# Optimization experiments

Measured on AMD Instinct MI355X. Metric: run time of the kernel, lower is better.

The kernel has to match this reference:

```python
import jax, jax.numpy as jnp
import numpy as np

NH = 16  # num_heads from init_kwargs


def setup_inputs() -> dict:
    key = jax.random.key(0)
    ks = jax.random.split(key, 7)
    B, L, S, H = 4, 2, 1024, 1024
    s = 0.02  # weight init scale to keep logits numerically tame
    return {
        "x": jax.random.normal(ks[0], (B, S, H), jnp.float32),
        "y": jax.random.normal(ks[1], (L, B, S, H), jnp.float32),
        "bias": jax.random.normal(ks[2], (B, 1, 1, S), jnp.float32),
        "Wq": jax.random.normal(ks[3], (H, H), jnp.float32) * s,
        "Wk": jax.random.normal(ks[4], (L, H, H), jnp.float32) * s,
        "Wv": jax.random.normal(ks[5], (L, H, H), jnp.float32) * s,
        "Wo": jax.random.normal(ks[6], (H, H), jnp.float32) * s,
    }


def reference(x, y, bias, Wq, Wk, Wv, Wo):
    # x: [B, Lq, H]; y: [L, B, Lk, H] (stacked list of per-link memories)
    B, Lq, H = x.shape
    L, _, Lk, _ = y.shape
    d = H // NH

    # shared query projection, split heads: [B, NH, Lq, d], pre-scaled
    q = (x @ Wq).reshape(B, Lq, NH, d).transpose(0, 2, 1, 3) * (d ** -0.5)

    # per-link K/V projections, split heads -> [B, L, NH, Lk, d]
    kp = jnp.einsum('lbsh,lhe->lbse', y, Wk).reshape(L, B, Lk, NH, d).transpose(1, 0, 3, 2, 4)
    vp = jnp.einsum('lbsh,lhe->lbse', y, Wv).reshape(L, B, Lk, NH, d).transpose(1, 0, 3, 2, 4)

    # per-link logits [B, L, NH, Lq, Lk] + broadcast bias (concat across links == broadcast)
    logits = jnp.einsum('bhqd,blhkd->blhqk', q, kp) + bias[:, None]

    # computation_mode == 1: joint softmax over the link-summed logits
    joint = logits.sum(axis=1)                # [B, NH, Lq, Lk]
    w = jax.nn.softmax(joint, axis=-1)        # (training=False -> no dropout)

    # sum_l (w @ v_l) == w @ sum_l v_l  (w is shared across links)
    ctx = jnp.einsum('bhqk,bhkd->bhqd', w, vp.sum(axis=1))

    # combine heads [B, Lq, H] and output projection
    out = ctx.transpose(0, 2, 1, 3).reshape(B, Lq, H) @ Wo
    return out
```

## Files before the change

### kernel.cpp

```cpp
#include <hip/hip_runtime.h>
#include <cstdint>

typedef __bf16 bf16_t;
typedef bf16_t bf16x4 __attribute__((ext_vector_type(4)));
typedef bf16_t bf16x8 __attribute__((ext_vector_type(8)));
typedef float f32x4 __attribute__((ext_vector_type(4)));

#define GLD_LDS16(g, l)                                                        \
  __builtin_amdgcn_global_load_lds(                                            \
      (const __attribute__((address_space(1))) void*)(g),                      \
      (__attribute__((address_space(3))) void*)(l), 16, 0, 0)

#define LOG2E 1.44269504088896340736f

static __device__ __forceinline__ unsigned short bf16_bits(float f) {
  bf16_t h = (bf16_t)f;
  return __builtin_bit_cast(unsigned short, h);
}

__global__ void prep_kernel(const float* __restrict__ x,
                            const float* __restrict__ y,
                            const float* __restrict__ Wq,
                            const float* __restrict__ Wk,
                            const float* __restrict__ Wv,
                            const float* __restrict__ Wo,
                            bf16_t* __restrict__ xb, bf16_t* __restrict__ yb,
                            bf16_t* __restrict__ WqT,
                            bf16_t* __restrict__ WkvT,
                            bf16_t* __restrict__ WoT) {
  __shared__ float tile[32][33];
  int bid = blockIdx.x;
  if (bid < 6144) {
    int i = bid * 256 + threadIdx.x;
    const float* src;
    bf16_t* dst;
    if (i < 524288) { src = x; dst = xb; }
    else            { src = y; dst = yb; i -= 524288; }
    const float4* s = (const float4*)src;
    float4 a = s[i * 2];
    float4 b = s[i * 2 + 1];
    bf16x8 o;
    o[0] = (bf16_t)a.x; o[1] = (bf16_t)a.y; o[2] = (bf16_t)a.z; o[3] = (bf16_t)a.w;
    o[4] = (bf16_t)b.x; o[5] = (bf16_t)b.y; o[6] = (bf16_t)b.z; o[7] = (bf16_t)b.w;
    *(bf16x8*)(dst + (size_t)i * 8) = o;
    return;
  }
  bid -= 6144;
  const float* src; bf16_t* dst; int R, lb;
  if (bid < 1024)      { src = Wq; dst = WqT;                        R = 1024; lb = bid; }
  else if (bid < 3072) { src = Wk; dst = WkvT;                       R = 2048; lb = bid - 1024; }
  else if (bid < 5120) { src = Wv; dst = WkvT + (size_t)1024 * 2048; R = 2048; lb = bid - 3072; }
  else                 { src = Wo; dst = WoT;                        R = 1024; lb = bid - 5120; }
  int c0 = (lb & 31) << 5, r0 = (lb >> 5) << 5;
  int tc = threadIdx.x & 31, tr = threadIdx.x >> 5;
#pragma unroll
  for (int i = 0; i < 4; i++)
    tile[tr + i * 8][tc] = src[(size_t)(r0 + tr + i * 8) * 1024 + c0 + tc];
  __syncthreads();
#pragma unroll
  for (int i = 0; i < 4; i++)
    dst[(size_t)(c0 + tr + i * 8) * R + r0 + tc] = (bf16_t)tile[tc][tr + i * 8];
}


#define GEMM_STAGE(buf, kt)                                                    \
  {                                                                            \
    const int kbase = (kt) * 32;                                               \
    int kg0 = kbase + ak0;                                                     \
    const bf16_t* s0 = (kg0 < Ksplit)                                          \
                           ? (A0 + (size_t)(m0 + ar0) * 1024 + kg0)            \
                           : (A1 + (size_t)(m0 + ar0) * 1024 + (kg0 - Ksplit));\
    GLD_LDS16(s0, As[buf] + c0 * 8);                                           \
    int kg1 = kbase + ak1;                                                     \
    const bf16_t* s1 = (kg1 < Ksplit)                                          \
                           ? (A0 + (size_t)(m0 + ar1) * 1024 + kg1)            \
                           : (A1 + (size_t)(m0 + ar1) * 1024 + (kg1 - Ksplit));\
    GLD_LDS16(s1, As[buf] + c1 * 8);                                           \
    const bf16_t* b0 = BT + (size_t)(n0 + ar0) * Ktot + kbase + ak0;           \
    GLD_LDS16(b0, Bs[buf] + c0 * 8);                                           \
    const bf16_t* b1 = BT + (size_t)(n0 + ar1) * Ktot + kbase + ak1;           \
    GLD_LDS16(b1, Bs[buf] + c1 * 8);                                           \
  }

#define GEMM_DECLS                                                             \
  const int t = threadIdx.x, w = t >> 6, l = t & 63;                           \
  const int l15 = l & 15, l4 = l >> 4;                                         \
  const int wr = w >> 1, wc = w & 1;                                           \
  const int c0 = t, c1 = t + 256;                                              \
  const int ar0 = c0 >> 2, ar1 = c1 >> 2;                                      \
  const int ak0 = ((c0 & 3) ^ ((ar0 >> 1) & 3)) * 8;                           \
  const int ak1 = ((c1 & 3) ^ ((ar1 >> 1) & 3)) * 8;                           \
  int offA[4], offB[4];                                                        \
  _Pragma("unroll") for (int mi = 0; mi < 4; mi++) {                           \
    int rA = wr * 64 + mi * 16 + l15;                                          \
    offA[mi] = rA * 32 + (l4 ^ ((rA >> 1) & 3)) * 8;                           \
    int rB = wc * 64 + mi * 16 + l15;                                          \
    offB[mi] = rB * 32 + (l4 ^ ((rB >> 1) & 3)) * 8;                           \
  }

#define GEMM_MAINLOOP                                                          \
  GEMM_STAGE(0, 0);                                                            \
  __syncthreads();                                                             \
  int cur = 0;                                                                 \
  for (int kt = 0; kt < nkt; ++kt) {                                           \
    if (kt + 1 < nkt) GEMM_STAGE(cur ^ 1, kt + 1);                             \
    bf16x8 af[4], bfr[4];                                                      \
    _Pragma("unroll") for (int mi = 0; mi < 4; mi++)                           \
        af[mi] = *(const bf16x8*)&As[cur][offA[mi]];                           \
    _Pragma("unroll") for (int ni = 0; ni < 4; ni++)                           \
        bfr[ni] = *(const bf16x8*)&Bs[cur][offB[ni]];                          \
    _Pragma("unroll") for (int mi = 0; mi < 4; mi++)                           \
        _Pragma("unroll") for (int ni = 0; ni < 4; ni++)                       \
            acc[mi][ni] = __builtin_amdgcn_mfma_f32_16x16x32_bf16(             \
                af[mi], bfr[ni], acc[mi][ni], 0, 0, 0);                        \
    __syncthreads();                                                           \
    cur ^= 1;                                                                  \
  }

__global__ __launch_bounds__(256, 2) void qkv_kernel(
    const bf16_t* __restrict__ xbp, const bf16_t* __restrict__ ybp,
    const bf16_t* __restrict__ WqT, const bf16_t* __restrict__ WkvT,
    bf16_t* __restrict__ Qb, bf16_t* __restrict__ Kb,
    bf16_t* __restrict__ VTb) {
  __shared__ bf16_t As[2][128 * 32];
  __shared__ bf16_t Bs[2][128 * 32];
  GEMM_DECLS
  const bool isQ = blockIdx.x < 256;
  const int i = isQ ? blockIdx.x : blockIdx.x - 256;
  const int ybt = (i & 7) * 4 + ((i >> 3) & 3);
  const int xbt = i >> 5;
  const int m0 = ybt * 128, n0 = xbt * 128;
  const bf16_t* A0 = isQ ? xbp : ybp;
  const bf16_t* A1 = isQ ? xbp : ybp + (size_t)4096 * 1024;
  const int Ksplit = 1024;
  const bf16_t* BT = isQ ? WqT : WkvT;
  const int Ktot = isQ ? 1024 : 2048;
  const int nkt = Ktot >> 5;
  f32x4 acc[4][4] = {};

  GEMM_MAINLOOP

#pragma unroll
  for (int mi = 0; mi < 4; mi++) {
#pragma unroll
    for (int ni = 0; ni < 4; ni++) {
      const int rbase = m0 + wr * 64 + mi * 16 + l4 * 4;
      const int col = n0 + wc * 64 + ni * 16 + l15;
      if (isQ) {
#pragma unroll
        for (int rr = 0; rr < 4; rr++)
          Qb[(size_t)(rbase + rr) * 1024 + col] =
              (bf16_t)(acc[mi][ni][rr] * (0.125f * LOG2E));
      } else if (n0 < 1024) {
#pragma unroll
        for (int rr = 0; rr < 4; rr++)
          Kb[(size_t)(rbase + rr) * 1024 + col] = (bf16_t)acc[mi][ni][rr];
      } else {
        union { unsigned short u[4]; uint2 v; } pk;
#pragma unroll
        for (int rr = 0; rr < 4; rr++)
          pk.u[rr] = bf16_bits(acc[mi][ni][rr]);
        *(uint2*)&VTb[(size_t)(col - 1024) * 4096 + rbase] = pk.v;
      }
    }
  }
}

__global__ __launch_bounds__(256, 2) void gemm_o(const bf16_t* __restrict__ A0,
                                                 const bf16_t* __restrict__ BT,
                                                 float* __restrict__ Cp) {
  __shared__ bf16_t As[2][128 * 32];
  __shared__ bf16_t Bs[2][128 * 32];
  GEMM_DECLS
  const int i = blockIdx.x;
  const int ybt = (i & 7) * 4 + ((i >> 3) & 3);
  const int xbt = i >> 5;
  const int m0 = ybt * 128, n0 = xbt * 128;
  const bf16_t* A1 = A0;
  const int Ksplit = 1024, Ktot = 1024, nkt = 32;
  f32x4 acc[4][4] = {};

  GEMM_MAINLOOP

#pragma unroll
  for (int mi = 0; mi < 4; mi++) {
#pragma unroll
    for (int ni = 0; ni < 4; ni++) {
      const int rbase = m0 + wr * 64 + mi * 16 + l4 * 4;
      const int col = n0 + wc * 64 + ni * 16 + l15;
#pragma unroll
      for (int rr = 0; rr < 4; rr++)
        Cp[(size_t)(rbase + rr) * 1024 + col] = acc[mi][ni][rr];
    }
  }
}

__global__ __launch_bounds__(256, 4) void attn_kernel(
    const bf16_t* __restrict__ Q, const bf16_t* __restrict__ K,
    const bf16_t* __restrict__ VT, const float* __restrict__ bias,
    bf16_t* __restrict__ ctx) {
  __shared__ bf16_t Ks[2][64 * 64];
  __shared__ bf16_t Vs[2][64 * 64];
  __shared__ bf16_t Ps[4][1024];
  const int t = threadIdx.x, w = t >> 6, l = t & 63;
  const int l15 = l & 15, l4 = l >> 4;
  const int id = blockIdx.x;
  const int bh = id & 63, qt = id >> 6;
  const int b = bh >> 4, h = bh & 15;

  bf16x8 qf[2];
  {
    const bf16_t* Qb =
        Q + (size_t)(b * 1024 + qt * 64 + w * 16 + l15) * 1024 + h * 64;
#pragma unroll
    for (int ks = 0; ks < 2; ks++)
      qf[ks] = *(const bf16x8*)&Qb[ks * 32 + l4 * 8];
  }

#define ATTN_STAGE(buf, kt)                                                    \
  {                                                                            \
    _Pragma("unroll") for (int j = 0; j < 2; j++) {                            \
      int c = t + j * 256;                                                     \
      int row = c >> 3, sl = (c & 7) ^ (row & 7);                              \
      const bf16_t* srck =                                                     \
          K + (size_t)(b * 1024 + (kt) * 64 + row) * 1024 + h * 64 + sl * 8;   \
      GLD_LDS16(srck, Ks[buf] + c * 8);                                        \
      const bf16_t* srcv =                                                     \
          VT + (size_t)(h * 64 + row) * 4096 + b * 1024 + (kt) * 64 + sl * 8;  \
      GLD_LDS16(srcv, Vs[buf] + c * 8);                                        \
    }                                                                          \
  }

  float mrun = -INFINITY, lrun = 0.f;
  f32x4 ctxacc[4] = {};

  ATTN_STAGE(0, 0);
  __syncthreads();
  int cur = 0;
  for (int kt = 0; kt < 16; ++kt) {
    if (kt + 1 < 16) ATTN_STAGE(cur ^ 1, kt + 1);

    f32x4 sacc[4] = {};
#pragma unroll
    for (int ks = 0; ks < 2; ks++) {
#pragma unroll
      for (int ni = 0; ni < 4; ni++) {
        int krow = ni * 16 + l15;
        int eoff = (krow * 64 + ks * 32 + l4 * 8) ^ ((krow & 7) << 3);
        bf16x8 kf = *(const bf16x8*)&Ks[cur][eoff];
        sacc[ni] = __builtin_amdgcn_mfma_f32_16x16x32_bf16(kf, qf[ks],
                                                           sacc[ni], 0, 0, 0);
      }
    }
#pragma unroll
    for (int ni = 0; ni < 4; ni++) {
      float4 bb =
          *(const float4*)&bias[b * 1024 + kt * 64 + ni * 16 + l4 * 4];
      sacc[ni][0] += (2.0f * LOG2E) * bb.x;
      sacc[ni][1] += (2.0f * LOG2E) * bb.y;
      sacc[ni][2] += (2.0f * LOG2E) * bb.z;
      sacc[ni][3] += (2.0f * LOG2E) * bb.w;
    }
    float tm = -INFINITY;
#pragma unroll
    for (int ni = 0; ni < 4; ni++)
#pragma unroll
      for (int rr = 0; rr < 4; rr++) tm = fmaxf(tm, sacc[ni][rr]);
    tm = fmaxf(tm, __shfl_xor(tm, 16));
    tm = fmaxf(tm, __shfl_xor(tm, 32));
    float mnew = fmaxf(mrun, tm);
    float sc = exp2f(mrun - mnew);
    float rsum = 0.f;
#pragma unroll
    for (int ni = 0; ni < 4; ni++) {
      bf16x4 pk;
#pragma unroll
      for (int rr = 0; rr < 4; rr++) {
        float p = exp2f(sacc[ni][rr] - mnew);
        rsum += p;
        pk[rr] = (bf16_t)p;
      }
      *(bf16x4*)&Ps[w][(ni * 2 + (l4 >> 1)) * 128 + l15 * 8 + (l4 & 1) * 4] =
          pk;
    }
    rsum += __shfl_xor(rsum, 16);
    rsum += __shfl_xor(rsum, 32);
    lrun = lrun * sc + rsum;
    mrun = mnew;
#pragma unroll
    for (int ni = 0; ni < 4; ni++) ctxacc[ni] *= sc;
#pragma unroll
    for (int kk = 0; kk < 2; kk++) {
      bf16x8 pf = *(const bf16x8*)&Ps[w][(kk * 4 + l4) * 128 + l15 * 8];
#pragma unroll
      for (int ni = 0; ni < 4; ni++) {
        int drow = ni * 16 + l15;
        int voff = (drow * 64 + kk * 32 + l4 * 8) ^ ((drow & 7) << 3);
        bf16x8 vf = *(const bf16x8*)&Vs[cur][voff];
        ctxacc[ni] = __builtin_amdgcn_mfma_f32_16x16x32_bf16(vf, pf, ctxacc[ni],
                                                             0, 0, 0);
      }
    }
    __syncthreads();
    cur ^= 1;
  }

  bf16_t* T = Ks[0];
  {
    float inv = 1.0f / lrun;
    int q = w * 16 + l15;
#pragma unroll
    for (int ni = 0; ni < 4; ni++) {
      bf16x4 tv;
#pragma unroll
      for (int rr = 0; rr < 4; rr++) tv[rr] = (bf16_t)(ctxacc[ni][rr] * inv);
      int d0 = ni * 16 + l4 * 4;
      *(bf16x4*)&T[q * 64 + (d0 ^ ((l15 & 7) << 3))] = tv;
    }
  }
  __syncthreads();
#pragma unroll
  for (int c = t; c < 512; c += 256) {
    int row = c >> 3, col8 = c & 7;
    bf16x8 v = *(const bf16x8*)&T[row * 64 + ((col8 * 8) ^ ((row & 7) << 3))];
    *(bf16x8*)&ctx[(size_t)(b * 1024 + qt * 64 + row) * 1024 + h * 64 +
                   col8 * 8] = v;
  }
#undef ATTN_STAGE
}

extern "C" void kernel_launch(void* const* d_in, const int* in_sizes, int n_in,
                              void* d_out, int out_size, void* d_ws,
                              size_t ws_size, hipStream_t stream) {
  const float* x = (const float*)d_in[0];
  const float* y = (const float*)d_in[1];
  const float* bias = (const float*)d_in[2];
  const float* Wq = (const float*)d_in[3];
  const float* Wk = (const float*)d_in[4];
  const float* Wv = (const float*)d_in[5];
  const float* Wo = (const float*)d_in[6];
  float* out = (float*)d_out;

  char* ws = (char*)d_ws;
  const size_t MB = 1024 * 1024;
  bf16_t* xb   = (bf16_t*)(ws + 0 * MB);
  bf16_t* yb   = (bf16_t*)(ws + 8 * MB);
  bf16_t* WqT  = (bf16_t*)(ws + 24 * MB);
  bf16_t* WkvT = (bf16_t*)(ws + 26 * MB);
  bf16_t* WoT  = (bf16_t*)(ws + 34 * MB);
  bf16_t* Qb   = (bf16_t*)(ws + 36 * MB);
  bf16_t* Kb   = (bf16_t*)(ws + 44 * MB);
  bf16_t* VTb  = (bf16_t*)(ws + 52 * MB);
  bf16_t* ctxb = (bf16_t*)(ws + 60 * MB);

  prep_kernel<<<12288, 256, 0, stream>>>(x, y, Wq, Wk, Wv, Wo, xb, yb, WqT,
                                         WkvT, WoT);
  qkv_kernel<<<768, 256, 0, stream>>>(xb, yb, WqT, WkvT, Qb, Kb, VTb);
  attn_kernel<<<1024, 256, 0, stream>>>(Qb, Kb, VTb, bias, ctxb);
  gemm_o<<<256, 256, 0, stream>>>(ctxb, WoT, out);
}
```

Baseline: 137.8 us.

## Switch attention to 32x32x16 MFMA with register-resident P via permlane swap

Rewrites the attention kernel to use 32x32x16 bf16 MFMA tiles, with each wave handling 32 query rows and a block covering 128 queries, so the grid is halved. The softmax probabilities are packed to bf16 with v_cvt_pk_bf16_f32 and rearranged across lane halves with v_permlane32_swap. This removes the LDS round trip for P and the extra shuffles for the row max and sum. The trade-off is higher register pressure (launch bounds lowered to 2 blocks) and fewer blocks in flight.

Measured after the change: 141.6 us. +2.7%, slower.

```diff
diff --git a/kernel.cpp b/kernel.cpp
--- a/kernel.cpp
+++ b/kernel.cpp
@@ -5,6 +5,7 @@
 typedef bf16_t bf16x4 __attribute__((ext_vector_type(4)));
 typedef bf16_t bf16x8 __attribute__((ext_vector_type(8)));
 typedef float f32x4 __attribute__((ext_vector_type(4)));
+typedef float f32x16 __attribute__((ext_vector_type(16)));
 
 #define GLD_LDS16(g, l)                                                        \
   __builtin_amdgcn_global_load_lds(                                            \
@@ -62,7 +63,6 @@
     dst[(size_t)(c0 + tr + i * 8) * R + r0 + tc] = (bf16_t)tile[tc][tr + i * 8];
 }
 
-
 #define GEMM_STAGE(buf, kt)                                                    \
   {                                                                            \
     const int kbase = (kt) * 32;                                               \
@@ -195,26 +195,25 @@
   }
 }
 
-__global__ __launch_bounds__(256, 4) void attn_kernel(
+__global__ __launch_bounds__(256, 2) void attn_kernel(
     const bf16_t* __restrict__ Q, const bf16_t* __restrict__ K,
     const bf16_t* __restrict__ VT, const float* __restrict__ bias,
     bf16_t* __restrict__ ctx) {
   __shared__ bf16_t Ks[2][64 * 64];
   __shared__ bf16_t Vs[2][64 * 64];
-  __shared__ bf16_t Ps[4][1024];
   const int t = threadIdx.x, w = t >> 6, l = t & 63;
-  const int l15 = l & 15, l4 = l >> 4;
+  const int l31 = l & 31, hi = l >> 5;
   const int id = blockIdx.x;
   const int bh = id & 63, qt = id >> 6;
   const int b = bh >> 4, h = bh & 15;
-
-  bf16x8 qf[2];
+  const int q_local = w * 32 + l31;
+
+  bf16x8 qf[4];
   {
-    const bf16_t* Qb =
-        Q + (size_t)(b * 1024 + qt * 64 + w * 16 + l15) * 1024 + h * 64;
-#pragma unroll
-    for (int ks = 0; ks < 2; ks++)
-      qf[ks] = *(const bf16x8*)&Qb[ks * 32 + l4 * 8];
+    const bf16_t* Qp =
+        Q + (size_t)(b * 1024 + qt * 128 + q_local) * 1024 + h * 64 + hi * 8;
+#pragma unroll
+    for (int ds = 0; ds < 4; ds++) qf[ds] = *(const bf16x8*)&Qp[ds * 16];
   }
 
 #define ATTN_STAGE(buf, kt)                                                    \
@@ -232,7 +231,7 @@
   }
 
   float mrun = -INFINITY, lrun = 0.f;
-  f32x4 ctxacc[4] = {};
+  f32x16 cacc[2] = {};
 
   ATTN_STAGE(0, 0);
   __syncthreads();
@@ -240,90 +239,117 @@
   for (int kt = 0; kt < 16; ++kt) {
     if (kt + 1 < 16) ATTN_STAGE(cur ^ 1, kt + 1);
 
-    f32x4 sacc[4] = {};
-#pragma unroll
-    for (int ks = 0; ks < 2; ks++) {
-#pragma unroll
-      for (int ni = 0; ni < 4; ni++) {
-        int krow = ni * 16 + l15;
-        int eoff = (krow * 64 + ks * 32 + l4 * 8) ^ ((krow & 7) << 3);
+    f32x16 sacc[2] = {};
+#pragma unroll
+    for (int ds = 0; ds < 4; ds++) {
+#pragma unroll
+      for (int kg = 0; kg < 2; kg++) {
+        int krow = kg * 32 + l31;
+        int eoff = (krow * 64 + ds * 16 + hi * 8) ^ ((krow & 7) << 3);
         bf16x8 kf = *(const bf16x8*)&Ks[cur][eoff];
-        sacc[ni] = __builtin_amdgcn_mfma_f32_16x16x32_bf16(kf, qf[ks],
-                                                           sacc[ni], 0, 0, 0);
-      }
-    }
-#pragma unroll
-    for (int ni = 0; ni < 4; ni++) {
-      float4 bb =
-          *(const float4*)&bias[b * 1024 + kt * 64 + ni * 16 + l4 * 4];
-      sacc[ni][0] += (2.0f * LOG2E) * bb.x;
-      sacc[ni][1] += (2.0f * LOG2E) * bb.y;
-      sacc[ni][2] += (2.0f * LOG2E) * bb.z;
-      sacc[ni][3] += (2.0f * LOG2E) * bb.w;
+        sacc[kg] = __builtin_amdgcn_mfma_f32_32x32x16_bf16(kf, qf[ds],
+                                                           sacc[kg], 0, 0, 0);
+      }
+    }
+#pragma unroll
+    for (int kg = 0; kg < 2; kg++) {
+#pragma unroll
+      for (int mm = 0; mm < 4; mm++) {
+        f32x4 bb = *(const f32x4*)&bias[b * 1024 + kt * 64 + kg * 32 + mm * 8 +
+                                        hi * 4];
+#pragma unroll
+        for (int rr = 0; rr < 4; rr++)
+          sacc[kg][mm * 4 + rr] += (2.0f * LOG2E) * bb[rr];
+      }
     }
     float tm = -INFINITY;
 #pragma unroll
-    for (int ni = 0; ni < 4; ni++)
-#pragma unroll
-      for (int rr = 0; rr < 4; rr++) tm = fmaxf(tm, sacc[ni][rr]);
-    tm = fmaxf(tm, __shfl_xor(tm, 16));
+    for (int kg = 0; kg < 2; kg++)
+#pragma unroll
+      for (int r = 0; r < 16; r++) tm = fmaxf(tm, sacc[kg][r]);
     tm = fmaxf(tm, __shfl_xor(tm, 32));
     float mnew = fmaxf(mrun, tm);
     float sc = exp2f(mrun - mnew);
     float rsum = 0.f;
 #pragma unroll
-    for (int ni = 0; ni < 4; ni++) {
-      bf16x4 pk;
-#pragma unroll
-      for (int rr = 0; rr < 4; rr++) {
-        float p = exp2f(sacc[ni][rr] - mnew);
+    for (int kg = 0; kg < 2; kg++)
+#pragma unroll
+      for (int r = 0; r < 16; r++) {
+        float p = exp2f(sacc[kg][r] - mnew);
+        sacc[kg][r] = p;
         rsum += p;
-        pk[rr] = (bf16_t)p;
-      }
-      *(bf16x4*)&Ps[w][(ni * 2 + (l4 >> 1)) * 128 + l15 * 8 + (l4 & 1) * 4] =
-          pk;
-    }
-    rsum += __shfl_xor(rsum, 16);
+      }
     rsum += __shfl_xor(rsum, 32);
     lrun = lrun * sc + rsum;
     mrun = mnew;
 #pragma unroll
-    for (int ni = 0; ni < 4; ni++) ctxacc[ni] *= sc;
-#pragma unroll
-    for (int kk = 0; kk < 2; kk++) {
-      bf16x8 pf = *(const bf16x8*)&Ps[w][(kk * 4 + l4) * 128 + l15 * 8];
-#pragma unroll
-      for (int ni = 0; ni < 4; ni++) {
-        int drow = ni * 16 + l15;
-        int voff = (drow * 64 + kk * 32 + l4 * 8) ^ ((drow & 7) << 3);
-        bf16x8 vf = *(const bf16x8*)&Vs[cur][voff];
-        ctxacc[ni] = __builtin_amdgcn_mfma_f32_16x16x32_bf16(vf, pf, ctxacc[ni],
-                                                             0, 0, 0);
+    for (int dg = 0; dg < 2; dg++)
+#pragma unroll
+      for (int r = 0; r < 16; r++) cacc[dg][r] *= sc;
+
+    bf16x8 pb[4];
+#pragma unroll
+    for (int kg = 0; kg < 2; kg++) {
+#pragma unroll
+      for (int tt = 0; tt < 2; tt++) {
+        uint32_t w0A, w1A, w0B, w1B;
+        const int mA = 2 * tt, mB = 2 * tt + 1;
+        asm("v_cvt_pk_bf16_f32 %0, %1, %2"
+            : "=v"(w0A)
+            : "v"(sacc[kg][4 * mA + 0]), "v"(sacc[kg][4 * mA + 1]));
+        asm("v_cvt_pk_bf16_f32 %0, %1, %2"
+            : "=v"(w1A)
+            : "v"(sacc[kg][4 * mA + 2]), "v"(sacc[kg][4 * mA + 3]));
+        asm("v_cvt_pk_bf16_f32 %0, %1, %2"
+            : "=v"(w0B)
+            : "v"(sacc[kg][4 * mB + 0]), "v"(sacc[kg][4 * mB + 1]));
+        asm("v_cvt_pk_bf16_f32 %0, %1, %2"
+            : "=v"(w1B)
+            : "v"(sacc[kg][4 * mB + 2]), "v"(sacc[kg][4 * mB + 3]));
+        asm("v_permlane32_swap_b32 %0, %1" : "+v"(w0A), "+v"(w0B));
+        asm("v_permlane32_swap_b32 %0, %1" : "+v"(w1A), "+v"(w1B));
+        union { uint32_t u[4]; bf16x8 v; } pk;
+        pk.u[0] = w0A; pk.u[1] = w1A; pk.u[2] = w0B; pk.u[3] = w1B;
+        pb[kg * 2 + tt] = pk.v;
+      }
+    }
+#pragma unroll
+    for (int dg = 0; dg < 2; dg++) {
+#pragma unroll
+      for (int k4 = 0; k4 < 4; k4++) {
+        int vrow = dg * 32 + l31;
+        int eoff = (vrow * 64 + k4 * 16 + hi * 8) ^ ((vrow & 7) << 3);
+        bf16x8 vf = *(const bf16x8*)&Vs[cur][eoff];
+        cacc[dg] = __builtin_amdgcn_mfma_f32_32x32x16_bf16(vf, pb[k4],
+                                                           cacc[dg], 0, 0, 0);
       }
     }
     __syncthreads();
     cur ^= 1;
   }
 
-  bf16_t* T = Ks[0];
+  bf16_t* T = (bf16_t*)Ks;
   {
     float inv = 1.0f / lrun;
-    int q = w * 16 + l15;
-#pragma unroll
-    for (int ni = 0; ni < 4; ni++) {
-      bf16x4 tv;
-#pragma unroll
-      for (int rr = 0; rr < 4; rr++) tv[rr] = (bf16_t)(ctxacc[ni][rr] * inv);
-      int d0 = ni * 16 + l4 * 4;
-      *(bf16x4*)&T[q * 64 + (d0 ^ ((l15 & 7) << 3))] = tv;
+#pragma unroll
+    for (int dg = 0; dg < 2; dg++) {
+#pragma unroll
+      for (int m = 0; m < 4; m++) {
+        bf16x4 tv;
+#pragma unroll
+        for (int rr = 0; rr < 4; rr++)
+          tv[rr] = (bf16_t)(cacc[dg][4 * m + rr] * inv);
+        int d0 = dg * 32 + m * 8 + hi * 4;
+        *(bf16x4*)&T[q_local * 64 + (d0 ^ ((q_local & 7) << 3))] = tv;
+      }
     }
   }
   __syncthreads();
 #pragma unroll
-  for (int c = t; c < 512; c += 256) {
+  for (int c = t; c < 1024; c += 256) {
     int row = c >> 3, col8 = c & 7;
     bf16x8 v = *(const bf16x8*)&T[row * 64 + ((col8 * 8) ^ ((row & 7) << 3))];
-    *(bf16x8*)&ctx[(size_t)(b * 1024 + qt * 64 + row) * 1024 + h * 64 +
+    *(bf16x8*)&ctx[(size_t)(b * 1024 + qt * 128 + row) * 1024 + h * 64 +
                    col8 * 8] = v;
   }
 #undef ATTN_STAGE
@@ -356,6 +382,6 @@
   prep_kernel<<<12288, 256, 0, stream>>>(x, y, Wq, Wk, Wv, Wo, xb, yb, WqT,
                                          WkvT, WoT);
   qkv_kernel<<<768, 256, 0, stream>>>(xb, yb, WqT, WkvT, Qb, Kb, VTb);
-  attn_kernel<<<1024, 256, 0, stream>>>(Qb, Kb, VTb, bias, ctxb);
+  attn_kernel<<<512, 256, 0, stream>>>(Qb, Kb, VTb, bias, ctxb);
   gemm_o<<<256, 256, 0, stream>>>(ctxb, WoT, out);
 }
```
